# Performance work log

Measured on AMD Instinct MI355X. Metric: run time of the kernel, lower is better.

Reference implementation:

```python
import jax, jax.numpy as jnp
import numpy as np

ORDER = 2
BN_EPS = 1e-5

def setup_inputs() -> dict:
    key = jax.random.key(0)
    ks = jax.random.split(key, 8)
    B, N, L, H = 32, 512, 12, 64
    S = 2                      # support_len
    OUT = 64                   # out_dim
    M = ORDER * S * H          # einsum middle dim = 256
    x = jax.random.normal(ks[0], (B, N, L, H), dtype=jnp.float32)
    # row-scaled random diffusion matrices to keep multi-hop propagation stable
    support = jax.random.uniform(ks[1], (S, N, N), dtype=jnp.float32) / N
    scale = 1.0 / M
    weight = scale * jax.random.normal(ks[2], (L, M, OUT), dtype=jnp.float32)
    eps = jnp.zeros((1,), dtype=jnp.float32)
    gamma = jnp.ones((OUT,), dtype=jnp.float32)
    beta = jnp.zeros((OUT,), dtype=jnp.float32)
    w2 = jax.random.normal(ks[3], (OUT, OUT), dtype=jnp.float32) / np.sqrt(OUT)
    b2 = jnp.zeros((OUT,), dtype=jnp.float32)
    return {"x": x, "support": support, "weight": weight, "eps": eps,
            "gamma": gamma, "beta": beta, "w2": w2, "b2": b2}

def reference(x, support, weight, eps, gamma, beta, w2, b2):
    B, N, L, H = x.shape
    xv = x.reshape(B, N, L * H)            # [B,N,LH]
    res = []
    for i in range(support.shape[0]):      # small fixed loop over supports
        A = support[i]                     # [N,N]
        out = xv
        for _ in range(ORDER):
            out = (1.0 + eps) * out + jnp.einsum('nm,bmd->bnd', A, out)
            res.append(out)
    out = jnp.stack(res, axis=-1)          # [B,N,LH,K], K = order*support_len
    K = out.shape[-1]
    out = out.reshape(B, N, L, H * K)      # [B,N,L,M]
    out = jnp.einsum('bnlm,lmo->bno', out, weight)   # [B,N,OUT]
    # dropout is identity in eval mode
    C = out.shape[-1]
    flat = out.reshape(B * N, C)
    mean = flat.mean(axis=0)
    var = flat.var(axis=0)                 # biased, matching torch BN training
    normed = (flat - mean) * jax.lax.rsqrt(var + BN_EPS) * gamma + beta
    y = jax.nn.relu(normed.reshape(B, N, C))
    return jnp.einsum('bnc,oc->bno', y, w2) + b2
```

## Files before the change

kernel.cpp:

```cpp
#include <hip/hip_runtime.h>
#include <hip/hip_bf16.h>
#include <cstddef>
#include <cstdint>

#define B_   32
#define N_   512
#define D_   768
#define OUT_ 64
#define R_   (B_ * N_)

typedef unsigned short u16;
typedef __bf16 bf16x8 __attribute__((ext_vector_type(8)));
typedef float  f32x4  __attribute__((ext_vector_type(4)));
typedef unsigned short u16x8 __attribute__((ext_vector_type(8)));

__device__ __forceinline__ u16 f2bf(float f) {
    __hip_bfloat16 h = __float2bfloat16(f);
    return __builtin_bit_cast(u16, h);
}

__device__ __forceinline__ f32x4 mfma16(u16x8 a, u16x8 b, f32x4 c) {
    return __builtin_amdgcn_mfma_f32_16x16x32_bf16(
        __builtin_bit_cast(bf16x8, a), __builtin_bit_cast(bf16x8, b), c, 0, 0, 0);
}

__device__ __forceinline__ void gl2lds16(const void* g, void* l) {
    __builtin_amdgcn_global_load_lds(
        (const __attribute__((address_space(1))) unsigned int*)g,
        (__attribute__((address_space(3))) unsigned int*)l, 16, 0, 0);
}

__global__ __launch_bounds__(256) void prep2(
    const float* __restrict__ support, const float* __restrict__ weight,
    const float* __restrict__ epsp,
    u16* __restrict__ MallC, u16* __restrict__ MT, u16* __restrict__ Wt)
{
    const int blk = blockIdx.x, tid = threadIdx.x;
    __shared__ float t[32][33];
    if (blk < 512) {
        int s = blk >> 8, rem = blk & 255;
        int n0 = (rem >> 4) * 32, m0 = (rem & 15) * 32;
        const float f = 1.0f + epsp[0];
        const float* S = support + (size_t)s * 262144;
#pragma unroll
        for (int p = 0; p < 4; ++p) {
            int nl = p * 8 + (tid >> 5), ml = tid & 31;
            float v = S[(size_t)(n0 + nl) * 512 + m0 + ml];
            if (n0 + nl == m0 + ml) v += f;
            MallC[(size_t)(n0 + nl) * 2048 + s * 1024 + m0 + ml] = f2bf(v);
            t[nl][ml] = v;
        }
        __syncthreads();
#pragma unroll
        for (int p = 0; p < 4; ++p) {
            int ml = p * 8 + (tid >> 5), nl = tid & 31;
            MT[(size_t)s * 262144 + (size_t)(m0 + ml) * 512 + n0 + nl] = f2bf(t[nl][ml]);
        }
    } else {
        int idx = (blk - 512) * 256 + tid;
        int k = idx / 49152, rem = idx % 49152;
        int o = rem / 768, d = rem % 768;
        int l = d >> 6, hh = d & 63;
        Wt[idx] = f2bf(weight[((size_t)l * 256 + hh * 4 + k) * 64 + o]);
    }
}

__global__ __launch_bounds__(256, 4) void zmsq(
    const u16* __restrict__ Wt, const float* __restrict__ x,
    const u16* __restrict__ MallC_in, const u16* __restrict__ MT,
    u16* __restrict__ Z, u16* __restrict__ MallC_out)
{
    __shared__ __align__(16) u16 SM[8192];
    const int tid = threadIdx.x, lane = tid & 63, wid = tid >> 6;
    const int wr = wid >> 1, wc = wid & 1;
    const int lrow = lane & 15, lk8 = (lane >> 4) * 8;
    const int q = lane >> 4;
    const int bid = blockIdx.x;

    f32x4 acc[2][2] = {};

    if (bid < 1024) {
        const int k = (bid >> 3) & 3;
        const int r2 = (bid >> 5) * 8 + (bid & 7);
        const int b = r2 >> 3, m0 = (r2 & 7) * 64;

        const u16* gsrcA[2]; u16* ldstA[2];
#pragma unroll
        for (int t = 0; t < 2; ++t) {
            int idx = wid * 2 + t;
            int p = idx >> 2, sub = idx & 3;
            gsrcA[t] = Wt + (size_t)(k * 64 + sub * 16 + lrow) * 768 + p * 32 + lk8;
            ldstA[t] = SM + p * 2048 + sub * 512;
        }
        const int r = tid >> 2, c4 = tid & 3;
        const float* gx = x + (size_t)(b * 512 + m0 + r) * 768 + c4 * 16;
        u16* bdst = SM + 4096 + (c4 >> 1) * 2048 + (r >> 4) * 512
                  + (c4 & 1) * 256 + (r & 15) * 8;

        for (int kk = 0; kk < 12; ++kk) {
#pragma unroll
            for (int t = 0; t < 2; ++t) gl2lds16(gsrcA[t], ldstA[t]);
#pragma unroll
            for (int t = 0; t < 2; ++t) gsrcA[t] += 64;
            f32x4 a0 = *(const f32x4*)(gx);
            f32x4 a1 = *(const f32x4*)(gx + 4);
            f32x4 a2 = *(const f32x4*)(gx + 8);
            f32x4 a3 = *(const f32x4*)(gx + 12);
            gx += 64;
            u16x8 w0, w1;
#pragma unroll
            for (int j = 0; j < 4; ++j) {
                w0[j] = f2bf(a0[j]); w0[4 + j] = f2bf(a1[j]);
                w1[j] = f2bf(a2[j]); w1[4 + j] = f2bf(a3[j]);
            }
            *(u16x8*)(bdst)       = w0;
            *(u16x8*)(bdst + 128) = w1;
            __syncthreads();
#pragma unroll
            for (int p = 0; p < 2; ++p) {
                u16x8 af[2], bq[2];
#pragma unroll
                for (int f = 0; f < 2; ++f)
                    af[f] = *(const u16x8*)(SM + p * 2048 + (wr * 2 + f) * 512 + lane * 8);
#pragma unroll
                for (int f = 0; f < 2; ++f)
                    bq[f] = *(const u16x8*)(SM + 4096 + p * 2048 + (wc * 2 + f) * 512 + lane * 8);
#pragma unroll
                for (int fi = 0; fi < 2; ++fi)
#pragma unroll
                    for (int fj = 0; fj < 2; ++fj)
                        acc[fi][fj] = mfma16(af[fi], bq[fj], acc[fi][fj]);
            }
            __syncthreads();
        }
        u16* Rw = SM + wid * 1280;
#pragma unroll
        for (int fi = 0; fi < 2; ++fi)
#pragma unroll
            for (int fj = 0; fj < 2; ++fj)
#pragma unroll
                for (int rr = 0; rr < 4; ++rr)
                    Rw[(fi * 16 + q * 4 + rr) * 40 + fj * 16 + lrow] = f2bf(acc[fi][fj][rr]);
        __syncthreads();
        const int r3 = lane >> 1, cc = (lane & 1) * 16;
        u16x8 v0 = *(const u16x8*)(Rw + r3 * 40 + cc);
        u16x8 v1 = *(const u16x8*)(Rw + r3 * 40 + cc + 8);
        u16* zp = Z + (size_t)(b * 64 + wr * 32 + r3) * 2048 + k * 512 + m0 + wc * 32 + cc;
        *(u16x8*)(zp)     = v0;
        *(u16x8*)(zp + 8) = v1;
    } else {
        const int lb = bid - 1024;
        const int s = lb >> 6, i0 = ((lb >> 3) & 7) * 64, j0 = (lb & 7) * 64;

        const u16* gsrc[4]; u16* ldst[4];
#pragma unroll
        for (int t = 0; t < 4; ++t) {
            int idx = wid * 4 + t;
            if (idx < 8) {
                int p = idx >> 2, sub = idx & 3;
                gsrc[t] = MallC_in + (size_t)(i0 + sub * 16 + lrow) * 2048 + s * 1024 + p * 32 + lk8;
                ldst[t] = SM + p * 2048 + sub * 512;
            } else {
                int i2 = idx - 8;
                int p = i2 >> 2, sub = i2 & 3;
                gsrc[t] = MT + (size_t)s * 262144 + (size_t)(j0 + sub * 16 + lrow) * 512 + p * 32 + lk8;
                ldst[t] = SM + 4096 + p * 2048 + sub * 512;
            }
        }
        for (int kk = 0; kk < 8; ++kk) {
#pragma unroll
            for (int t = 0; t < 4; ++t) gl2lds16(gsrc[t], ldst[t]);
#pragma unroll
            for (int t = 0; t < 4; ++t) gsrc[t] += 64;
            __syncthreads();
#pragma unroll
            for (int p = 0; p < 2; ++p) {
                u16x8 af[2], bq[2];
#pragma unroll
                for (int f = 0; f < 2; ++f)
                    af[f] = *(const u16x8*)(SM + p * 2048 + (wr * 2 + f) * 512 + lane * 8);
#pragma unroll
                for (int f = 0; f < 2; ++f)
                    bq[f] = *(const u16x8*)(SM + 4096 + p * 2048 + (wc * 2 + f) * 512 + lane * 8);
#pragma unroll
                for (int fi = 0; fi < 2; ++fi)
#pragma unroll
                    for (int fj = 0; fj < 2; ++fj)
                        acc[fi][fj] = mfma16(af[fi], bq[fj], acc[fi][fj]);
            }
            __syncthreads();
        }
#pragma unroll
        for (int fi = 0; fi < 2; ++fi)
#pragma unroll
            for (int fj = 0; fj < 2; ++fj)
#pragma unroll
                for (int rr = 0; rr < 4; ++rr) {
                    int n = i0 + wr * 32 + fi * 16 + q * 4 + rr;
                    int c = j0 + wc * 32 + fj * 16 + lrow;
                    MallC_out[(size_t)n * 2048 + (2 * s + 1) * 512 + c] = f2bf(acc[fi][fj][rr]);
                }
    }
}

__global__ __launch_bounds__(256, 4) void ysum(
    const u16* __restrict__ G, const u16* __restrict__ Z, float* __restrict__ Yh)
{
    __shared__ __align__(16) u16 SM[8192];
    const int tid = threadIdx.x, lane = tid & 63, wid = tid >> 6;
    const int wr = wid >> 1, wc = wid & 1;
    const int lrow = lane & 15, lk8 = (lane >> 4) * 8;
    const int bid = blockIdx.x;
    const int kq = bid >> 8, rt = bid & 255;
    const int r0 = rt * 64, b = rt >> 3, n0 = r0 & 511;

    const u16* gsrc[4]; u16* ldst[4];
#pragma unroll
    for (int t = 0; t < 4; ++t) {
        int idx = wid * 4 + t;
        if (idx < 8) {
            int p = idx >> 2, sub = idx & 3;
            gsrc[t] = G + (size_t)(n0 + sub * 16 + lrow) * 2048 + kq * 512 + p * 32 + lk8;
            ldst[t] = SM + p * 2048 + sub * 512;
        } else {
            int i2 = idx - 8;
            int p = i2 >> 2, sub = i2 & 3;
            gsrc[t] = Z + (size_t)(b * 64 + sub * 16 + lrow) * 2048 + kq * 512 + p * 32 + lk8;
            ldst[t] = SM + 4096 + p * 2048 + sub * 512;
        }
    }
    f32x4 acc[2][2] = {};
    for (int kk = 0; kk < 8; ++kk) {
#pragma unroll
        for (int t = 0; t < 4; ++t) gl2lds16(gsrc[t], ldst[t]);
#pragma unroll
        for (int t = 0; t < 4; ++t) gsrc[t] += 64;
        __syncthreads();
#pragma unroll
        for (int p = 0; p < 2; ++p) {
            u16x8 af[2], bq[2];
#pragma unroll
            for (int f = 0; f < 2; ++f)
                af[f] = *(const u16x8*)(SM + p * 2048 + (wr * 2 + f) * 512 + lane * 8);
#pragma unroll
            for (int f = 0; f < 2; ++f)
                bq[f] = *(const u16x8*)(SM + 4096 + p * 2048 + (wc * 2 + f) * 512 + lane * 8);
#pragma unroll
            for (int fi = 0; fi < 2; ++fi)
#pragma unroll
                for (int fj = 0; fj < 2; ++fj)
                    acc[fi][fj] = mfma16(af[fi], bq[fj], acc[fi][fj]);
        }
        __syncthreads();
    }
    const int q = lane >> 4;
    float* Yk = Yh + (size_t)kq * R_ * 64;
#pragma unroll
    for (int fi = 0; fi < 2; ++fi)
#pragma unroll
        for (int fj = 0; fj < 2; ++fj)
#pragma unroll
            for (int rr = 0; rr < 4; ++rr) {
                int r2 = r0 + wr * 32 + fi * 16 + q * 4 + rr;
                int o  = wc * 32 + fj * 16 + lrow;
                Yk[(size_t)r2 * 64 + o] = acc[fi][fj][rr];
            }
}

__global__ __launch_bounds__(256) void bn_part(
    const float* __restrict__ Yh, float* __restrict__ part)
{
    const int blk = blockIdx.x, tid = threadIdx.x;
    const int o = tid & 63, g = tid >> 6;
    float s = 0.f, s2 = 0.f;
#pragma unroll
    for (int p = 0; p < 16; ++p) {
        int r = blk * 64 + p * 4 + g;
        size_t off = (size_t)r * 64 + o;
        float v = Yh[off] + Yh[(size_t)R_ * 64 + off]
                + Yh[(size_t)2 * R_ * 64 + off] + Yh[(size_t)3 * R_ * 64 + off];
        s += v; s2 += v * v;
    }
    __shared__ float ls[4][64], ls2[4][64];
    ls[g][o] = s; ls2[g][o] = s2;
    __syncthreads();
    if (tid < 64) {
        float t = 0.f, t2 = 0.f;
#pragma unroll
        for (int g2 = 0; g2 < 4; ++g2) { t += ls[g2][tid]; t2 += ls2[g2][tid]; }
        part[blk * 128 + tid]      = t;
        part[blk * 128 + 64 + tid] = t2;
    }
}

__global__ __launch_bounds__(256) void bn_out(
    const float* __restrict__ Yh, const float* __restrict__ part,
    const float* __restrict__ gamma, const float* __restrict__ beta,
    const float* __restrict__ w2, const float* __restrict__ b2,
    float* __restrict__ out)
{
    __shared__ float ys[64 * 68];
    __shared__ float w2s[64 * 65];
    __shared__ float red[4][64], red2[4][64];
    __shared__ float sa[64], sh[64];
    const int tid = threadIdx.x;
    const int r0 = blockIdx.x * 64;
    const int o = tid & 63, g = tid >> 6;
    {
        float s = 0.f, s2 = 0.f;
        for (int p = g; p < 256; p += 4) {
            s  += part[p * 128 + o];
            s2 += part[p * 128 + 64 + o];
        }
        red[g][o] = s; red2[g][o] = s2;
    }
#pragma unroll
    for (int i = 0; i < 16; ++i) {
        int idx = tid + i * 256;
        w2s[(idx >> 6) * 65 + (idx & 63)] = w2[idx];
    }
    __syncthreads();
    if (tid < 64) {
        float t0 = red[0][tid] + red[1][tid] + red[2][tid] + red[3][tid];
        float t2 = red2[0][tid] + red2[1][tid] + red2[2][tid] + red2[3][tid];
        float mean = t0 * (1.0f / R_);
        float var  = t2 * (1.0f / R_) - mean * mean;
        float a = rsqrtf(var + 1e-5f) * gamma[tid];
        sa[tid] = a;
        sh[tid] = beta[tid] - mean * a;
    }
    __syncthreads();
    {
        float a = sa[o], bsh = sh[o];
#pragma unroll
        for (int p = 0; p < 16; ++p) {
            int rl = p * 4 + g;
            size_t off = (size_t)(r0 + rl) * 64 + o;
            float v = Yh[off] + Yh[(size_t)R_ * 64 + off]
                    + Yh[(size_t)2 * R_ * 64 + off] + Yh[(size_t)3 * R_ * 64 + off];
            ys[o * 68 + rl] = fmaxf(fmaf(v, a, bsh), 0.f);
        }
    }
    __syncthreads();
    float acc[16];
    float bb = b2[o];
#pragma unroll
    for (int j = 0; j < 16; ++j) acc[j] = bb;
    for (int c = 0; c < 64; ++c) {
        float wv = w2s[o * 65 + c];
        const float* yr = ys + c * 68 + g * 16;
        f32x4 y0 = *(const f32x4*)(yr);
        f32x4 y1 = *(const f32x4*)(yr + 4);
        f32x4 y2 = *(const f32x4*)(yr + 8);
        f32x4 y3 = *(const f32x4*)(yr + 12);
#pragma unroll
        for (int j = 0; j < 4; ++j) {
            acc[j]      = fmaf(wv, y0[j], acc[j]);
            acc[4 + j]  = fmaf(wv, y1[j], acc[4 + j]);
            acc[8 + j]  = fmaf(wv, y2[j], acc[8 + j]);
            acc[12 + j] = fmaf(wv, y3[j], acc[12 + j]);
        }
    }
#pragma unroll
    for (int j = 0; j < 16; ++j)
        out[(size_t)(r0 + g * 16 + j) * OUT_ + o] = acc[j];
}

extern "C" void kernel_launch(void* const* d_in, const int* in_sizes, int n_in,
                              void* d_out, int out_size, void* d_ws, size_t ws_size,
                              hipStream_t stream)
{
    const float* x       = (const float*)d_in[0];
    const float* support = (const float*)d_in[1];
    const float* weight  = (const float*)d_in[2];
    const float* eps     = (const float*)d_in[3];
    const float* gamma   = (const float*)d_in[4];
    const float* beta    = (const float*)d_in[5];
    const float* w2      = (const float*)d_in[6];
    const float* b2      = (const float*)d_in[7];
    float* out = (float*)d_out;

    char* ws = (char*)d_ws;
    u16*   MallC = (u16*)(ws);
    u16*   MT    = (u16*)(ws + 2097152);
    u16*   Wt    = (u16*)(ws + 3145728);
    u16*   Z     = (u16*)(ws + 3538944);
    float* Yh    = (float*)(ws + 11927552);
    float* part  = (float*)(ws + 28704768);

    prep2  <<<1280, 256, 0, stream>>>(support, weight, eps, MallC, MT, Wt);
    zmsq   <<<1152, 256, 0, stream>>>(Wt, x, MallC, MT, Z, MallC);
    ysum   <<<1024, 256, 0, stream>>>(MallC, Z, Yh);
    bn_part<<<256,  256, 0, stream>>>(Yh, part);
    bn_out <<<256,  256, 0, stream>>>(Yh, part, gamma, beta, w2, b2, out);
}
```

Measured before the change: 171.8 us.

## Double-buffer LDS tiles in zmsq and ysum GEMM loops

After: 168.3 us. 1.02x faster.

```diff
diff --git a/kernel.cpp b/kernel.cpp
--- a/kernel.cpp
+++ b/kernel.cpp
@@ -70,7 +70,7 @@
     const u16* __restrict__ MallC_in, const u16* __restrict__ MT,
     u16* __restrict__ Z, u16* __restrict__ MallC_out)
 {
-    __shared__ __align__(16) u16 SM[8192];
+    __shared__ __align__(16) u16 SM[16384];
     const int tid = threadIdx.x, lane = tid & 63, wid = tid >> 6;
     const int wr = wid >> 1, wc = wid & 1;
     const int lrow = lane & 15, lk8 = (lane >> 4) * 8;
@@ -97,16 +97,13 @@
         u16* bdst = SM + 4096 + (c4 >> 1) * 2048 + (r >> 4) * 512
                   + (c4 & 1) * 256 + (r & 15) * 8;
 
-        for (int kk = 0; kk < 12; ++kk) {
-#pragma unroll
-            for (int t = 0; t < 2; ++t) gl2lds16(gsrcA[t], ldstA[t]);
-#pragma unroll
-            for (int t = 0; t < 2; ++t) gsrcA[t] += 64;
+        {
             f32x4 a0 = *(const f32x4*)(gx);
             f32x4 a1 = *(const f32x4*)(gx + 4);
             f32x4 a2 = *(const f32x4*)(gx + 8);
             f32x4 a3 = *(const f32x4*)(gx + 12);
-            gx += 64;
+#pragma unroll
+            for (int t = 0; t < 2; ++t) gl2lds16(gsrcA[t], ldstA[t]);
             u16x8 w0, w1;
 #pragma unroll
             for (int j = 0; j < 4; ++j) {
@@ -115,21 +112,47 @@
             }
             *(u16x8*)(bdst)       = w0;
             *(u16x8*)(bdst + 128) = w1;
-            __syncthreads();
+        }
+        __syncthreads();
+
+#pragma unroll 2
+        for (int kk = 0; kk < 12; ++kk) {
+            const int cb = (kk & 1) * 8192, nb = cb ^ 8192;
+            f32x4 a0, a1, a2, a3;
+            if (kk < 11) {
+                const float* g = gx + (kk + 1) * 64;
+                a0 = *(const f32x4*)(g);
+                a1 = *(const f32x4*)(g + 4);
+                a2 = *(const f32x4*)(g + 8);
+                a3 = *(const f32x4*)(g + 12);
+#pragma unroll
+                for (int t = 0; t < 2; ++t)
+                    gl2lds16(gsrcA[t] + (kk + 1) * 64, ldstA[t] + nb);
+            }
 #pragma unroll
             for (int p = 0; p < 2; ++p) {
                 u16x8 af[2], bq[2];
 #pragma unroll
                 for (int f = 0; f < 2; ++f)
-                    af[f] = *(const u16x8*)(SM + p * 2048 + (wr * 2 + f) * 512 + lane * 8);
+                    af[f] = *(const u16x8*)(SM + cb + p * 2048 + (wr * 2 + f) * 512 + lane * 8);
 #pragma unroll
                 for (int f = 0; f < 2; ++f)
-                    bq[f] = *(const u16x8*)(SM + 4096 + p * 2048 + (wc * 2 + f) * 512 + lane * 8);
+                    bq[f] = *(const u16x8*)(SM + cb + 4096 + p * 2048 + (wc * 2 + f) * 512 + lane * 8);
 #pragma unroll
                 for (int fi = 0; fi < 2; ++fi)
 #pragma unroll
                     for (int fj = 0; fj < 2; ++fj)
                         acc[fi][fj] = mfma16(af[fi], bq[fj], acc[fi][fj]);
+            }
+            if (kk < 11) {
+                u16x8 w0, w1;
+#pragma unroll
+                for (int j = 0; j < 4; ++j) {
+                    w0[j] = f2bf(a0[j]); w0[4 + j] = f2bf(a1[j]);
+                    w1[j] = f2bf(a2[j]); w1[4 + j] = f2bf(a3[j]);
+                }
+                *(u16x8*)(bdst + nb)       = w0;
+                *(u16x8*)(bdst + nb + 128) = w1;
             }
             __syncthreads();
         }
@@ -167,21 +190,26 @@
                 ldst[t] = SM + 4096 + p * 2048 + sub * 512;
             }
         }
+#pragma unroll
+        for (int t = 0; t < 4; ++t) gl2lds16(gsrc[t], ldst[t]);
+        __syncthreads();
+#pragma unroll 2
         for (int kk = 0; kk < 8; ++kk) {
-#pragma unroll
-            for (int t = 0; t < 4; ++t) gl2lds16(gsrc[t], ldst[t]);
-#pragma unroll
-            for (int t = 0; t < 4; ++t) gsrc[t] += 64;
-            __syncthreads();
+            const int cb = (kk & 1) * 8192, nb = cb ^ 8192;
+            if (kk < 7) {
+#pragma unroll
+                for (int t = 0; t < 4; ++t)
+                    gl2lds16(gsrc[t] + (kk + 1) * 64, ldst[t] + nb);
+            }
 #pragma unroll
             for (int p = 0; p < 2; ++p) {
                 u16x8 af[2], bq[2];
 #pragma unroll
                 for (int f = 0; f < 2; ++f)
-                    af[f] = *(const u16x8*)(SM + p * 2048 + (wr * 2 + f) * 512 + lane * 8);
+                    af[f] = *(const u16x8*)(SM + cb + p * 2048 + (wr * 2 + f) * 512 + lane * 8);
 #pragma unroll
                 for (int f = 0; f < 2; ++f)
-                    bq[f] = *(const u16x8*)(SM + 4096 + p * 2048 + (wc * 2 + f) * 512 + lane * 8);
+                    bq[f] = *(const u16x8*)(SM + cb + 4096 + p * 2048 + (wc * 2 + f) * 512 + lane * 8);
 #pragma unroll
                 for (int fi = 0; fi < 2; ++fi)
 #pragma unroll
@@ -206,7 +234,7 @@
 __global__ __launch_bounds__(256, 4) void ysum(
     const u16* __restrict__ G, const u16* __restrict__ Z, float* __restrict__ Yh)
 {
-    __shared__ __align__(16) u16 SM[8192];
+    __shared__ __align__(16) u16 SM[16384];
     const int tid = threadIdx.x, lane = tid & 63, wid = tid >> 6;
     const int wr = wid >> 1, wc = wid & 1;
     const int lrow = lane & 15, lk8 = (lane >> 4) * 8;
@@ -230,21 +258,26 @@
         }
     }
     f32x4 acc[2][2] = {};
+#pragma unroll
+    for (int t = 0; t < 4; ++t) gl2lds16(gsrc[t], ldst[t]);
+    __syncthreads();
+#pragma unroll 2
     for (int kk = 0; kk < 8; ++kk) {
-#pragma unroll
-        for (int t = 0; t < 4; ++t) gl2lds16(gsrc[t], ldst[t]);
-#pragma unroll
-        for (int t = 0; t < 4; ++t) gsrc[t] += 64;
-        __syncthreads();
+        const int cb = (kk & 1) * 8192, nb = cb ^ 8192;
+        if (kk < 7) {
+#pragma unroll
+            for (int t = 0; t < 4; ++t)
+                gl2lds16(gsrc[t] + (kk + 1) * 64, ldst[t] + nb);
+        }
 #pragma unroll
         for (int p = 0; p < 2; ++p) {
             u16x8 af[2], bq[2];
 #pragma unroll
             for (int f = 0; f < 2; ++f)
-                af[f] = *(const u16x8*)(SM + p * 2048 + (wr * 2 + f) * 512 + lane * 8);
+                af[f] = *(const u16x8*)(SM + cb + p * 2048 + (wr * 2 + f) * 512 + lane * 8);
 #pragma unroll
             for (int f = 0; f < 2; ++f)
-                bq[f] = *(const u16x8*)(SM + 4096 + p * 2048 + (wc * 2 + f) * 512 + lane * 8);
+                bq[f] = *(const u16x8*)(SM + cb + 4096 + p * 2048 + (wc * 2 + f) * 512 + lane * 8);
 #pragma unroll
             for (int fi = 0; fi < 2; ++fi)
 #pragma unroll
```
